# Optimization experiments

Measured on AMD Instinct MI355X. Metric: run time of the kernel, lower is better.

The kernel has to match this reference:

```python
import jax, jax.numpy as jnp
import numpy as np


def setup_inputs() -> dict:
    key = jax.random.key(0)
    k1, k2, k3, k4 = jax.random.split(key, 4)
    B, D, U = 16, 2048, 37
    inputs = jax.random.normal(k1, (B, D), dtype=jnp.float32)
    matrix = jax.random.normal(k2, (D, D), dtype=jnp.float32) * 0.05
    weight = jax.random.normal(k3, (U, D, D), dtype=jnp.float32) * 0.05
    bias = jax.random.normal(k4, (U,), dtype=jnp.float32) * 0.05
    return {"inputs": inputs, "matrix": matrix, "weight": weight, "bias": bias}


def reference(inputs, matrix, weight, bias):
    # inputs: (B, D); matrix: (D, D); weight: (U, D, D); bias: (U,)
    B, D = inputs.shape
    idx = jnp.arange(D)
    # maps = ones((B, D, D)) with per-row diagonal replaced by inputs[b]
    maps = jnp.ones((B, D, D), dtype=inputs.dtype).at[:, idx, idx].set(inputs)
    # masked multiply by learned matrix (broadcast over batch) then relu
    masked = jax.nn.relu(matrix[None, :, :] * maps)  # (B, D, D)
    # outer-product-then-reduce collapses to a direct contraction per unit:
    # conv[b, u] = sum_ij masked[b, i, j] * weight[u, i, j]
    conv = jnp.einsum('bij,uij->bu', masked, weight)
    return conv + bias[None, :]
```

## Files before the change

### kernel.cpp

```cpp
#include <hip/hip_runtime.h>

constexpr int BB = 16;
constexpr int D  = 2048;
constexpr int U  = 37;
constexpr long long DD = (long long)D * D;

constexpr int TPB = 256;
constexpr int C   = 1024;
constexpr int F4_PER_BLOCK  = (int)(DD / 4 / C);
constexpr int F4_PER_THREAD = F4_PER_BLOCK / TPB;
constexpr int NGRP = 5;


template<int G>
__device__ __forceinline__ void stream_group(
    const int u0, const int c, const long long base4,
    const float4 (&m)[F4_PER_THREAD],
    const float* __restrict__ weight,
    float* __restrict__ partial)
{
    float acc[G];
#pragma unroll
    for (int g = 0; g < G; ++g) acc[g] = 0.f;

#pragma unroll
    for (int g = 0; g < G; ++g) {
        const float4* __restrict__ w4 =
            (const float4*)(weight + (long long)(u0 + g) * DD);
#pragma unroll
        for (int it = 0; it < F4_PER_THREAD; ++it) {
            const float4 w = w4[base4 + (long long)it * TPB];
            acc[g] = fmaf(m[it].x, w.x, acc[g]);
            acc[g] = fmaf(m[it].y, w.y, acc[g]);
            acc[g] = fmaf(m[it].z, w.z, acc[g]);
            acc[g] = fmaf(m[it].w, w.w, acc[g]);
        }
    }

#pragma unroll
    for (int g = 0; g < G; ++g)
#pragma unroll
        for (int off = 32; off > 0; off >>= 1)
            acc[g] += __shfl_down(acc[g], off, 64);

    __shared__ float lpart[G];
    if (threadIdx.x < G) lpart[threadIdx.x] = 0.f;
    __syncthreads();
    if ((threadIdx.x & 63) == 0) {
#pragma unroll
        for (int g = 0; g < G; ++g)
            atomicAdd(&lpart[g], acc[g]);
    }
    __syncthreads();
    if (threadIdx.x < G)
        partial[(long long)(u0 + threadIdx.x) * C + c] = lpart[threadIdx.x];
}

__global__ __launch_bounds__(TPB, 4) void base_kernel(
    const float* __restrict__ matrix,
    const float* __restrict__ weight,
    float* __restrict__ partial,
    float* __restrict__ wdiag)
{
    const int grp = blockIdx.x;
    const int c   = blockIdx.y;
    const long long base4 = (long long)c * F4_PER_BLOCK + threadIdx.x;
    const float4* __restrict__ m4 = (const float4*)matrix;

    float4 m[F4_PER_THREAD];
#pragma unroll
    for (int it = 0; it < F4_PER_THREAD; ++it) {
        float4 t = m4[base4 + (long long)it * TPB];
        m[it].x = fmaxf(t.x, 0.f);
        m[it].y = fmaxf(t.y, 0.f);
        m[it].z = fmaxf(t.z, 0.f);
        m[it].w = fmaxf(t.w, 0.f);
    }

    if (grp == 0 && threadIdx.x < 2 * U) {
        const int u = threadIdx.x >> 1;
        const int i = 2 * c + (threadIdx.x & 1);
        wdiag[u * D + i] = weight[(long long)u * DD + (long long)i * (D + 1)];
    }

    if (grp < 4) stream_group<8>(grp * 8, c, base4, m, weight, partial);
    else         stream_group<5>(32,      c, base4, m, weight, partial);
}

__global__ __launch_bounds__(TPB) void finish_kernel(
    const float* __restrict__ inputs,
    const float* __restrict__ matrix,
    const float* __restrict__ bias,
    const float* __restrict__ partial,
    const float* __restrict__ wdiag,
    float* __restrict__ out)
{
    const int u = blockIdx.x;
    const int b = blockIdx.y;

    float acc = 0.f;
    for (int i = threadIdx.x; i < D; i += TPB) {
        float mm = matrix[(long long)i * (D + 1)];
        float wd = wdiag[u * D + i];
        float x  = inputs[b * D + i];
        acc += (fmaxf(mm * x, 0.f) - fmaxf(mm, 0.f)) * wd;
    }
    for (int cc = threadIdx.x; cc < C; cc += TPB)
        acc += partial[(long long)u * C + cc];

#pragma unroll
    for (int off = 32; off > 0; off >>= 1)
        acc += __shfl_down(acc, off, 64);

    __shared__ float smem[TPB / 64];
    if ((threadIdx.x & 63) == 0) smem[threadIdx.x >> 6] = acc;
    __syncthreads();
    if (threadIdx.x == 0) {
        float t = 0.f;
#pragma unroll
        for (int w = 0; w < TPB / 64; ++w) t += smem[w];
        out[b * U + u] = t + bias[u];
    }
}

extern "C" void kernel_launch(void* const* d_in, const int* in_sizes, int n_in,
                              void* d_out, int out_size, void* d_ws, size_t ws_size,
                              hipStream_t stream) {
    const float* inputs = (const float*)d_in[0];
    const float* matrix = (const float*)d_in[1];
    const float* weight = (const float*)d_in[2];
    const float* bias   = (const float*)d_in[3];
    float* out     = (float*)d_out;
    float* partial = (float*)d_ws;
    float* wdiag   = (float*)d_ws + (long long)U * C;

    base_kernel<<<dim3(NGRP, C), TPB, 0, stream>>>(matrix, weight, partial, wdiag);
    finish_kernel<<<dim3(U, BB), TPB, 0, stream>>>(inputs, matrix, bias,
                                                   partial, wdiag, out);
}
```

Before: 805.7 us.

## Double-buffer weight plane loads with nontemporal loads and larger per-block chunks

Halves the chunk count so each thread keeps 8 float4 of the matrix instead of 4. Weight planes are now loaded into two register buffers in ping-pong fashion, so the next unit's plane is in flight while the current one is accumulated. Loads use nontemporal hints to avoid polluting caches with the streamed weights, and the occupancy hint drops from 4 to 2 blocks per CU to make room for the extra registers. The wdiag extraction is adjusted to cover 4 rows per chunk. Fewer resident waves could reduce memory-level parallelism on this bandwidth-bound stream.

```diff
diff --git a/kernel.cpp b/kernel.cpp
--- a/kernel.cpp
+++ b/kernel.cpp
@@ -6,16 +6,37 @@
 constexpr long long DD = (long long)D * D;
 
 constexpr int TPB = 256;
-constexpr int C   = 1024;
-constexpr int F4_PER_BLOCK  = (int)(DD / 4 / C);
-constexpr int F4_PER_THREAD = F4_PER_BLOCK / TPB;
+constexpr int C   = 512;
+constexpr int F4B = (int)(DD / 4 / C);
+constexpr int F4T = F4B / TPB;
 constexpr int NGRP = 5;
 
+
+using f4 = __attribute__((ext_vector_type(4))) float;
+
+__device__ __forceinline__ void load_plane(f4 (&buf)[F4T],
+                                           const f4* __restrict__ w4,
+                                           const long long base4) {
+#pragma unroll
+    for (int it = 0; it < F4T; ++it)
+        buf[it] = __builtin_nontemporal_load(&w4[base4 + (long long)it * TPB]);
+}
+
+__device__ __forceinline__ void fma_plane(float& acc, const f4 (&m)[F4T],
+                                          const f4 (&buf)[F4T]) {
+#pragma unroll
+    for (int it = 0; it < F4T; ++it) {
+        acc = fmaf(m[it].x, buf[it].x, acc);
+        acc = fmaf(m[it].y, buf[it].y, acc);
+        acc = fmaf(m[it].z, buf[it].z, acc);
+        acc = fmaf(m[it].w, buf[it].w, acc);
+    }
+}
 
 template<int G>
 __device__ __forceinline__ void stream_group(
     const int u0, const int c, const long long base4,
-    const float4 (&m)[F4_PER_THREAD],
+    const f4 (&m)[F4T],
     const float* __restrict__ weight,
     float* __restrict__ partial)
 {
@@ -23,18 +44,18 @@
 #pragma unroll
     for (int g = 0; g < G; ++g) acc[g] = 0.f;
 
+    f4 bufA[F4T], bufB[F4T];
+    load_plane(bufA, (const f4*)(weight + (long long)u0 * DD), base4);
+
 #pragma unroll
-    for (int g = 0; g < G; ++g) {
-        const float4* __restrict__ w4 =
-            (const float4*)(weight + (long long)(u0 + g) * DD);
-#pragma unroll
-        for (int it = 0; it < F4_PER_THREAD; ++it) {
-            const float4 w = w4[base4 + (long long)it * TPB];
-            acc[g] = fmaf(m[it].x, w.x, acc[g]);
-            acc[g] = fmaf(m[it].y, w.y, acc[g]);
-            acc[g] = fmaf(m[it].z, w.z, acc[g]);
-            acc[g] = fmaf(m[it].w, w.w, acc[g]);
-        }
+    for (int g = 0; g < G; g += 2) {
+        if (g + 1 < G)
+            load_plane(bufB, (const f4*)(weight + (long long)(u0 + g + 1) * DD), base4);
+        fma_plane(acc[g], m, bufA);
+        if (g + 2 < G)
+            load_plane(bufA, (const f4*)(weight + (long long)(u0 + g + 2) * DD), base4);
+        if (g + 1 < G)
+            fma_plane(acc[g + 1], m, bufB);
     }
 
 #pragma unroll
@@ -56,7 +77,7 @@
         partial[(long long)(u0 + threadIdx.x) * C + c] = lpart[threadIdx.x];
 }
 
-__global__ __launch_bounds__(TPB, 4) void base_kernel(
+__global__ __launch_bounds__(TPB, 2) void base_kernel(
     const float* __restrict__ matrix,
     const float* __restrict__ weight,
     float* __restrict__ partial,
@@ -64,22 +85,22 @@
 {
     const int grp = blockIdx.x;
     const int c   = blockIdx.y;
-    const long long base4 = (long long)c * F4_PER_BLOCK + threadIdx.x;
-    const float4* __restrict__ m4 = (const float4*)matrix;
+    const long long base4 = (long long)c * F4B + threadIdx.x;
+    const f4* __restrict__ m4 = (const f4*)matrix;
 
-    float4 m[F4_PER_THREAD];
+    f4 m[F4T];
 #pragma unroll
-    for (int it = 0; it < F4_PER_THREAD; ++it) {
-        float4 t = m4[base4 + (long long)it * TPB];
+    for (int it = 0; it < F4T; ++it) {
+        f4 t = m4[base4 + (long long)it * TPB];
         m[it].x = fmaxf(t.x, 0.f);
         m[it].y = fmaxf(t.y, 0.f);
         m[it].z = fmaxf(t.z, 0.f);
         m[it].w = fmaxf(t.w, 0.f);
     }
 
-    if (grp == 0 && threadIdx.x < 2 * U) {
-        const int u = threadIdx.x >> 1;
-        const int i = 2 * c + (threadIdx.x & 1);
+    if (grp == 0 && threadIdx.x < 4 * U) {
+        const int u = threadIdx.x >> 2;
+        const int i = 4 * c + (threadIdx.x & 3);
         wdiag[u * D + i] = weight[(long long)u * DD + (long long)i * (D + 1)];
     }
 
```

Measured after the change: 784.0 us. 1.03x faster.
